# Kernel tuning notes

Measured on AMD Instinct MI355X. Metric: run time of the kernel, lower is better.

The kernel has to match this reference:

```python
import jax, jax.numpy as jnp
import numpy as np

S, Q, N, T, G = 20000, 32, 200000, 30, 64
D_IN, H, D_SV, D_LANG, D_FUSE = 300, 256, 64, 64, 128

def setup_inputs() -> dict:
    key = jax.random.key(0)
    ks = jax.random.split(key, 20)
    sc = 0.05
    inp = {
        'lang_feat': jax.random.normal(ks[0], (Q, T, D_IN), jnp.float32),
        'supvox_feat': jax.random.normal(ks[1], (S, D_SV), jnp.float32),
        'supvox_coords': jax.random.uniform(ks[2], (S, 3), jnp.float32),
        'lang_len': jax.random.randint(ks[3], (Q,), 5, T + 1).astype(jnp.int32),
        'grps': jax.random.randint(ks[4], (S,), 0, G).astype(jnp.int32),
        'supervox': jax.random.randint(ks[5], (N,), 0, S).astype(jnp.int32),
        'gt': jax.random.randint(ks[6], (N, Q), 0, 2).astype(jnp.int32),
        # GRU params (torch layout: [3H, in])
        'gru_w_ih': sc * jax.random.normal(ks[7], (3 * H, D_IN), jnp.float32),
        'gru_w_hh': sc * jax.random.normal(ks[8], (3 * H, H), jnp.float32),
        'gru_b_ih': sc * jax.random.normal(ks[9], (3 * H,), jnp.float32),
        'gru_b_hh': sc * jax.random.normal(ks[10], (3 * H,), jnp.float32),
        # lang_sqz: Linear(256,64) ReLU Linear(64,64)
        'sqz_w1': sc * jax.random.normal(ks[11], (D_LANG, H), jnp.float32),
        'sqz_b1': sc * jax.random.normal(ks[12], (D_LANG,), jnp.float32),
        'sqz_w2': sc * jax.random.normal(ks[13], (D_LANG, D_LANG), jnp.float32),
        'sqz_b2': sc * jax.random.normal(ks[14], (D_LANG,), jnp.float32),
        # feat_fuse: Linear(131,128) ReLU
        'fuse_w': sc * jax.random.normal(ks[15], (D_FUSE, D_SV + 3 + D_LANG), jnp.float32),
        'fuse_b': sc * jax.random.normal(ks[16], (D_FUSE,), jnp.float32),
        # heat_map: Linear(128,2) (Dropout = identity in eval)
        'heat_w': sc * jax.random.normal(ks[17], (2, D_FUSE), jnp.float32),
        'heat_b': sc * jax.random.normal(ks[18], (2,), jnp.float32),
    }
    return inp

def _gru_last(x, lens, w_ih, w_hh, b_ih, b_hh):
    # x: [Q, T, D_IN]; returns hidden at step lens[q]-1 (pack_padded_sequence semantics)
    def step(h, xt_t):
        xt, t = xt_t  # xt: [Q, D_IN]
        gi = xt @ w_ih.T + b_ih          # [Q, 3H]
        gh = h @ w_hh.T + b_hh           # [Q, 3H]
        ir, iz, inn = jnp.split(gi, 3, -1)
        hr, hz, hn = jnp.split(gh, 3, -1)
        r = jax.nn.sigmoid(ir + hr)
        z = jax.nn.sigmoid(iz + hz)
        n = jnp.tanh(inn + r * hn)
        h_new = (1.0 - z) * n + z * h
        h = jnp.where((t < lens)[:, None], h_new, h)
        return h, None
    h0 = jnp.zeros((x.shape[0], w_hh.shape[1]), x.dtype)
    hT, _ = jax.lax.scan(step, h0, (jnp.swapaxes(x, 0, 1), jnp.arange(x.shape[1])))
    return hT  # [Q, H]

def reference(lang_feat, supvox_feat, supvox_coords, lang_len, grps, supervox, gt,
              gru_w_ih, gru_w_hh, gru_b_ih, gru_b_hh,
              sqz_w1, sqz_b1, sqz_w2, sqz_b2, fuse_w, fuse_b, heat_w, heat_b):
    # language branch
    h = _gru_last(lang_feat, lang_len, gru_w_ih, gru_w_hh, gru_b_ih, gru_b_hh)  # [Q,H]
    lang = jax.nn.relu(h @ sqz_w1.T + sqz_b1) @ sqz_w2.T + sqz_b2               # [Q,64]
    # supervoxel branch: cat(feat, coords) -> [S,67]
    sv = jnp.concatenate([supvox_feat, supvox_coords], -1)
    # feat_fuse on cat(sv, lang): split the weight to avoid materializing [S,Q,131]
    d_sv = sv.shape[-1]
    sv_proj = sv @ fuse_w[:, :d_sv].T           # [S,128]
    lang_proj = lang @ fuse_w[:, d_sv:].T       # [Q,128]
    fused = jax.nn.relu(sv_proj[:, None, :] + lang_proj[None, :, :] + fuse_b)  # [S,Q,128]
    logits = fused @ heat_w.T + heat_b          # [S,Q,2]
    obj_score = jax.nn.softmax(logits, -1)[..., 1]  # [S,Q]
    # cluster-grouped mean score (grps_ one-hot; assumes unique(grps)==arange(G))
    grp_oh = (grps[:, None] == jnp.arange(G)).astype(obj_score.dtype)  # [S,G]
    grp_sum = jnp.einsum('sq,sg->qg', obj_score, grp_oh)               # [Q,G]
    sen_grp_score = grp_sum / grp_oh.sum(0)[None, :]                   # [Q,G]
    best = jnp.argmax(sen_grp_score, -1)        # [Q]
    supvox_sen = grp_oh[:, best]                # [S,Q] binary
    obj_pts = supvox_sen[supervox].astype(jnp.int32)  # [N,Q]
    inter = (obj_pts * gt).sum(0).astype(jnp.float32)
    union = jnp.bitwise_or(obj_pts, gt).sum(0).astype(jnp.float32)
    ious = inter / (union + 1e-5)               # [Q]
    return obj_pts, ious
```

## Files before the change

kernel.cpp:

```cpp
#include <hip/hip_runtime.h>
#include <hip/hip_bf16.h>
#include <math.h>

#define S_TOT 20000
#define Q_TOT 32
#define N_TOT 200000
#define T_MAX 30
#define G_TOT 64
#define D_IN 300
#define H_DIM 256
#define D_SV 64
#define D_LANG 64
#define D_FUSE 128
#define D_CAT 67
#define FW_LD 131
#define SCHUNK 32
#define NBLK3 (S_TOT / SCHUNK)
#define SENT64 0xFFFFFFFFFFFFFFFFull
#define PCHUNK 16
#define PTILES 40

#define GI_MT 32
#define GI_NT 64
#define GI_KC 100
#define GI_NB 12
#define GI_GRID (30 * GI_NB)
#define HG_ELEMS (30 * Q_TOT * H_DIM)

#define SYNCS_N 1024

__device__ __forceinline__ float sigmoidf_(float x) { return 1.0f / (1.0f + expf(-x)); }
__device__ __forceinline__ unsigned long long pack2(float a, float b) {
    return ((unsigned long long)__float_as_uint(b) << 32) | (unsigned long long)__float_as_uint(a);
}

__global__ __launch_bounds__(128) void k_gi(const float* __restrict__ lang_feat,
                                            const float* __restrict__ w_ih,
                                            const float* __restrict__ b_ih,
                                            const float* __restrict__ fuse_w,
                                            const float* __restrict__ sqz_w1,
                                            const float* __restrict__ sqz_w2,
                                            const float* __restrict__ heat_w,
                                            float* __restrict__ gi,
                                            float* __restrict__ fwt,
                                            float* __restrict__ w1t,
                                            float* __restrict__ w2t,
                                            float* __restrict__ wdr,
                                            float* __restrict__ hg,
                                            int* __restrict__ syncs) {
    const int tid = threadIdx.x;
    if (blockIdx.x >= GI_GRID) {
        const int xb = blockIdx.x - GI_GRID;
        if (xb == 0) {
            for (int i = tid; i < FW_LD * D_FUSE; i += 128)
                fwt[(i % FW_LD) * D_FUSE + (i / FW_LD)] = fuse_w[i];
            for (int i = tid; i < D_LANG * H_DIM; i += 128)
                w1t[(i & 255) * D_LANG + (i >> 8)] = sqz_w1[i];
            for (int i = tid; i < D_LANG * D_LANG; i += 128)
                w2t[(i & 63) * D_LANG + (i >> 6)] = sqz_w2[i];
            if (tid < D_FUSE) wdr[tid] = heat_w[D_FUSE + tid] - heat_w[tid];
        } else {
            const int fb = xb - 1;
            const int per4 = HG_ELEMS / 4 / 8;
            float4* dst = (float4*)hg + fb * per4;
            const float4 sv = make_float4(__uint_as_float(0xFFFFFFFFu), __uint_as_float(0xFFFFFFFFu),
                                          __uint_as_float(0xFFFFFFFFu), __uint_as_float(0xFFFFFFFFu));
            for (int i = tid; i < per4; i += 128) dst[i] = sv;
            if (fb == 0) for (int i = tid; i < SYNCS_N; i += 128) syncs[i] = 0;
        }
        return;
    }
    __shared__ float x_l[GI_KC][GI_MT + 1];
    __shared__ float w_l[GI_KC][GI_NT + 1];
    const int mb = blockIdx.x / GI_NB, nb = blockIdx.x % GI_NB;
    const int m0 = mb * GI_MT, n0 = nb * GI_NT;
    const int tq4 = (tid >> 4) * 4, jq4 = (tid & 15) * 4;

    float acc[4][4];
    #pragma unroll
    for (int i = 0; i < 4; ++i)
        #pragma unroll
        for (int j = 0; j < 4; ++j) acc[i][j] = 0.f;

    for (int kc = 0; kc < 3; ++kc) {
        const int k0 = kc * GI_KC;
        for (int i = tid; i < GI_MT * GI_KC; i += 128) {
            const int r = i / GI_KC, k = i % GI_KC;
            const int row = m0 + r, q = row / T_MAX, t = row - q * T_MAX;
            x_l[k][r] = lang_feat[(q * T_MAX + t) * D_IN + k0 + k];
        }
        for (int i = tid; i < GI_NT * GI_KC; i += 128) {
            const int r = i / GI_KC, k = i % GI_KC;
            w_l[k][r] = w_ih[(n0 + r) * D_IN + k0 + k];
        }
        __syncthreads();
        #pragma unroll 2
        for (int k = 0; k < GI_KC; ++k) {
            const float x0 = x_l[k][tq4 + 0], x1 = x_l[k][tq4 + 1];
            const float x2 = x_l[k][tq4 + 2], x3 = x_l[k][tq4 + 3];
            const float v0 = w_l[k][jq4 + 0], v1 = w_l[k][jq4 + 1];
            const float v2 = w_l[k][jq4 + 2], v3 = w_l[k][jq4 + 3];
            acc[0][0] = fmaf(x0, v0, acc[0][0]); acc[0][1] = fmaf(x0, v1, acc[0][1]);
            acc[0][2] = fmaf(x0, v2, acc[0][2]); acc[0][3] = fmaf(x0, v3, acc[0][3]);
            acc[1][0] = fmaf(x1, v0, acc[1][0]); acc[1][1] = fmaf(x1, v1, acc[1][1]);
            acc[1][2] = fmaf(x1, v2, acc[1][2]); acc[1][3] = fmaf(x1, v3, acc[1][3]);
            acc[2][0] = fmaf(x2, v0, acc[2][0]); acc[2][1] = fmaf(x2, v1, acc[2][1]);
            acc[2][2] = fmaf(x2, v2, acc[2][2]); acc[2][3] = fmaf(x2, v3, acc[2][3]);
            acc[3][0] = fmaf(x3, v0, acc[3][0]); acc[3][1] = fmaf(x3, v1, acc[3][1]);
            acc[3][2] = fmaf(x3, v2, acc[3][2]); acc[3][3] = fmaf(x3, v3, acc[3][3]);
        }
        __syncthreads();
    }
    const float b0 = b_ih[n0 + jq4 + 0], b1 = b_ih[n0 + jq4 + 1];
    const float b2 = b_ih[n0 + jq4 + 2], b3 = b_ih[n0 + jq4 + 3];
    #pragma unroll
    for (int i = 0; i < 4; ++i) {
        const int row = m0 + tq4 + i;
        const int q = row / T_MAX, t = row - q * T_MAX;
        float4 v = make_float4(acc[i][0] + b0, acc[i][1] + b1, acc[i][2] + b2, acc[i][3] + b3);
        *(float4*)&gi[(q * T_MAX + t) * 768 + n0 + jq4] = v;
    }
}

__global__ __launch_bounds__(384, 1) void k_gru8(const float* __restrict__ gi,
                                                 const float* __restrict__ w_hh,
                                                 const float* __restrict__ b_hh,
                                                 const int* __restrict__ lang_len,
                                                 float* __restrict__ hg,
                                                 float* __restrict__ hbuf,
                                                 const float* __restrict__ w1t,
                                                 const float* __restrict__ b1,
                                                 const float* __restrict__ w2t,
                                                 const float* __restrict__ b2,
                                                 const float* __restrict__ fwt,
                                                 const float* __restrict__ fuse_b,
                                                 float* __restrict__ langc,
                                                 int* __restrict__ qdone) {
    __shared__ __align__(16) float wlds[96 * 256];
    __shared__ __align__(16) float hlq[4 * 68];
    __shared__ float ghl[96];
    __shared__ float gil[T_MAX * 96];

    const int tid = threadIdx.x;
    const int q = blockIdx.x >> 3, b = blockIdx.x & 7;
    int len = lang_len[q]; if (len > T_MAX) len = T_MAX; if (len < 1) len = 1;

    {
        const float4* src4 = (const float4*)w_hh;
        float4* dst4 = (float4*)wlds;
        for (int i = tid; i < 96 * 64; i += 384) {
            const int r = i >> 6, c = i & 63;
            const int grow = ((r >> 5) << 8) + (b << 5) + (r & 31);
            dst4[r * 64 + (c ^ (r & 7))] = src4[grow * 64 + c];
        }
    }
    for (int i = tid; i < len * 96; i += 384) {
        const int t = i / 96, r = i % 96;
        gil[i] = gi[(q * T_MAX + t) * 768 + ((r >> 5) << 8) + (b << 5) + (r & 31)];
    }
    __syncthreads();

    float hfin = 0.f;
    {
        float hnew = 0.f;
        if (tid < 32) {
            const float bhr = b_hh[(b << 5) + tid];
            const float bhz = b_hh[H_DIM + (b << 5) + tid];
            const float bhn = b_hh[2 * H_DIM + (b << 5) + tid];
            const float r = sigmoidf_(gil[tid] + bhr);
            const float z = sigmoidf_(gil[32 + tid] + bhz);
            const float n = tanhf(gil[64 + tid] + r * bhn);
            hnew = (1.f - z) * n;
            if (len == 1) hfin = hnew;
        }
        if (tid < 64 && len > 1) {
            const float a0 = __shfl(hnew, 2 * (tid & 15));
            const float a1 = __shfl(hnew, 2 * (tid & 15) + 1);
            if (tid < 16) {
                unsigned long long* dst = (unsigned long long*)(hg + q * H_DIM + (b << 5));
                __hip_atomic_store(dst + tid, pack2(a0, a1), __ATOMIC_RELAXED, __HIP_MEMORY_SCOPE_AGENT);
            }
        }
    }

    const int row = tid >> 2, ql = tid & 3;
    const float bh = b_hh[((row >> 5) << 8) + (b << 5) + (row & 31)];
    const int rx = row & 7;
    const float4* wrow4 = (const float4*)wlds + row * 64;
    const int cbase = ql << 4;

    for (int t = 1; t < len; ++t) {
        if (tid < 128) {
            const unsigned long long* src =
                (const unsigned long long*)(hg + (size_t)(t - 1) * (Q_TOT * H_DIM) + q * H_DIM);
            unsigned long long v;
            while ((v = __hip_atomic_load(src + tid, __ATOMIC_RELAXED,
                                          __HIP_MEMORY_SCOPE_AGENT)) == SENT64)
                __builtin_amdgcn_s_sleep(1);
            const int k = 2 * tid;
            const int o = (k >> 6) * 68 + (k & 63);
            hlq[o]     = __uint_as_float((unsigned)(v & 0xffffffffu));
            hlq[o + 1] = __uint_as_float((unsigned)(v >> 32));
        }
        __syncthreads();
        float hold = 0.f;
        if (tid < 32) { const int k = (b << 5) + tid; hold = hlq[(k >> 6) * 68 + (k & 63)]; }
        const float4* h4 = (const float4*)(hlq + ql * 68);
        float ax = 0.f, ay = 0.f, az = 0.f, aw = 0.f;
        #pragma unroll
        for (int i = 0; i < 16; ++i) {
            const float4 wv = wrow4[(cbase + i) ^ rx];
            const float4 hv = h4[i];
            ax = fmaf(wv.x, hv.x, ax);
            ay = fmaf(wv.y, hv.y, ay);
            az = fmaf(wv.z, hv.z, az);
            aw = fmaf(wv.w, hv.w, aw);
        }
        float s = (ax + ay) + (az + aw);
        s += __shfl_xor(s, 1);
        s += __shfl_xor(s, 2);
        if (ql == 0) ghl[row] = s + bh;
        __syncthreads();
        float hnew = 0.f;
        if (tid < 32) {
            const float* gt_ = gil + t * 96;
            const float r = sigmoidf_(gt_[tid] + ghl[tid]);
            const float z = sigmoidf_(gt_[32 + tid] + ghl[32 + tid]);
            const float n = tanhf(gt_[64 + tid] + r * ghl[64 + tid]);
            hnew = (1.f - z) * n + z * hold;
            if (t == len - 1) hfin = hnew;
        }
        if (tid < 64 && t < len - 1) {
            const float a0 = __shfl(hnew, 2 * (tid & 15));
            const float a1 = __shfl(hnew, 2 * (tid & 15) + 1);
            if (tid < 16) {
                unsigned long long* dst =
                    (unsigned long long*)(hg + (size_t)t * (Q_TOT * H_DIM) + q * H_DIM + (b << 5));
                __hip_atomic_store(dst + tid, pack2(a0, a1), __ATOMIC_RELAXED, __HIP_MEMORY_SCOPE_AGENT);
            }
        }
    }

    if (tid < 32)
        __hip_atomic_store(&hbuf[q * H_DIM + (b << 5) + tid], hfin,
                           __ATOMIC_RELAXED, __HIP_MEMORY_SCOPE_AGENT);
    asm volatile("s_waitcnt vmcnt(0)" ::: "memory");
    __syncthreads();
    if (tid == 0)
        __hip_atomic_fetch_add(&qdone[q], 1, __ATOMIC_RELAXED, __HIP_MEMORY_SCOPE_AGENT);
    if (b != 0) return;

    if (tid == 0) {
        while (__hip_atomic_load(&qdone[q], __ATOMIC_RELAXED, __HIP_MEMORY_SCOPE_AGENT) < 8)
            __builtin_amdgcn_s_sleep(2);
    }
    __syncthreads();
    float* hql = gil;
    float* t1l = gil + 256;
    float* lgl = gil + 320;
    if (tid < H_DIM)
        hql[tid] = __hip_atomic_load(&hbuf[q * H_DIM + tid], __ATOMIC_RELAXED, __HIP_MEMORY_SCOPE_AGENT);
    __syncthreads();
    if (tid < 256) {
        const int c = tid >> 2, qq = tid & 3;
        float a = 0.f;
        #pragma unroll 8
        for (int j = 0; j < 64; ++j) {
            const int k = (qq << 6) + j;
            a = fmaf(w1t[k * D_LANG + c], hql[k], a);
        }
        a += __shfl_xor(a, 1);
        a += __shfl_xor(a, 2);
        if (qq == 0) t1l[c] = fmaxf(a + b1[c], 0.f);
    }
    __syncthreads();
    if (tid < 256) {
        const int c = tid >> 2, qq = tid & 3;
        float a = 0.f;
        #pragma unroll
        for (int j = 0; j < 16; ++j) {
            const int k = (qq << 4) + j;
            a = fmaf(w2t[k * D_LANG + c], t1l[k], a);
        }
        a += __shfl_xor(a, 1);
        a += __shfl_xor(a, 2);
        if (qq == 0) lgl[c] = a + b2[c];
    }
    __syncthreads();
    if (tid < 256) {
        const int d = tid >> 1, hh = tid & 1;
        float a = 0.f;
        #pragma unroll 8
        for (int j = 0; j < 32; ++j) {
            const int k = (hh << 5) + j;
            a = fmaf(fwt[(D_CAT + k) * D_FUSE + d], lgl[k], a);
        }
        a += __shfl_xor(a, 1);
        if (hh == 0) langc[q * D_FUSE + d] = a + fuse_b[d];
    }
}

__global__ __launch_bounds__(256, 3) void k_tail(const float* __restrict__ feat,
                                                 const float* __restrict__ coords,
                                                 const int* __restrict__ grps,
                                                 const float* __restrict__ langc,
                                                 const float* __restrict__ fwt,
                                                 const float* __restrict__ wdr_g,
                                                 const float* __restrict__ heat_b,
                                                 float* __restrict__ grp_part,
                                                 int* __restrict__ cnt_part,
                                                 float* __restrict__ grp2,
                                                 int* __restrict__ cnt2,
                                                 int* __restrict__ best,
                                                 const int* __restrict__ supervox,
                                                 const int* __restrict__ gt,
                                                 float* __restrict__ out,
                                                 int* __restrict__ syncs) {
    int* interG = syncs;
    int* unionG = syncs + 32;
    int* t_out  = syncs + 64;
    int* gtick  = syncs + 65;
    int* qtick  = syncs + 98;
    const int tid = threadIdx.x;
    const int bid = blockIdx.x;

    __shared__ __align__(16) float svin[SCHUNK][68];
    __shared__ __align__(16) float svp[SCHUNK][132];
    __shared__ float score[SCHUNK][Q_TOT];
    __shared__ int grps_l[SCHUNK];
    __shared__ float ps[4][G_TOT];
    __shared__ int   pc[4][G_TOT];
    __shared__ float sc[G_TOT];
    __shared__ int bl[Q_TOT];
    __shared__ int gm[G_TOT];
    __shared__ int bi_s[Q_TOT], bu_s[Q_TOT];
    __shared__ int islast;

    {
        const int s0 = bid * SCHUNK;
        const int dsl = tid & 7, q = tid >> 3;
        float lc[16], wdr[16];
        #pragma unroll
        for (int i = 0; i < 16; ++i) {
            const int d = dsl * 16 + i;
            lc[i]  = langc[q * D_FUSE + d];
            wdr[i] = wdr_g[d];
        }
        const float hbd = heat_b[1] - heat_b[0];

        for (int i = tid; i < SCHUNK * D_SV; i += 256) {
            const int r = i >> 6, c = i & 63;
            svin[r][c] = feat[(s0 + r) * D_SV + c];
        }
        if (tid < SCHUNK * 3) { const int r = tid / 3, c = tid % 3; svin[r][D_SV + c] = coords[(s0 + r) * 3 + c]; }
        if (tid < SCHUNK) grps_l[tid] = grps[s0 + tid];
        __syncthreads();

        {
            const int d = tid & 127, sl0 = tid >> 7;
            float acc[16];
            #pragma unroll
            for (int i = 0; i < 16; ++i) acc[i] = 0.f;
            for (int k4 = 0; k4 < 16; ++k4) {
                const float w0 = fwt[(4 * k4 + 0) * D_FUSE + d];
                const float w1 = fwt[(4 * k4 + 1) * D_FUSE + d];
                const float w2 = fwt[(4 * k4 + 2) * D_FUSE + d];
                const float w3 = fwt[(4 * k4 + 3) * D_FUSE + d];
                #pragma unroll
                for (int i = 0; i < 16; ++i) {
                    const float4 xv = *(const float4*)&svin[sl0 + 2 * i][4 * k4];
                    acc[i] = fmaf(xv.x, w0, fmaf(xv.y, w1, fmaf(xv.z, w2, fmaf(xv.w, w3, acc[i]))));
                }
            }
            for (int k = 64; k < D_CAT; ++k) {
                const float wv = fwt[k * D_FUSE + d];
                #pragma unroll
                for (int i = 0; i < 16; ++i)
                    acc[i] = fmaf(svin[sl0 + 2 * i][k], wv, acc[i]);
            }
            #pragma unroll
            for (int i = 0; i < 16; ++i) svp[sl0 + 2 * i][d] = acc[i];
        }
        __syncthreads();

        for (int sl = 0; sl < SCHUNK; ++sl) {
            const float4* sv4 = (const float4*)(&svp[sl][dsl * 16]);
            float part = 0.f;
            #pragma unroll
            for (int j = 0; j < 4; ++j) {
                const float4 v = sv4[j];
                part = fmaf(fmaxf(v.x + lc[4*j+0], 0.f), wdr[4*j+0], part);
                part = fmaf(fmaxf(v.y + lc[4*j+1], 0.f), wdr[4*j+1], part);
                part = fmaf(fmaxf(v.z + lc[4*j+2], 0.f), wdr[4*j+2], part);
                part = fmaf(fmaxf(v.w + lc[4*j+3], 0.f), wdr[4*j+3], part);
            }
            part += __shfl_xor(part, 1);
            part += __shfl_xor(part, 2);
            part += __shfl_xor(part, 4);
            if (dsl == 0) score[sl][q] = sigmoidf_(part + hbd);
        }
        __syncthreads();

        for (int i = 0; i < 8; ++i) {
            const int cell = tid + 256 * i;
            const int qq = cell >> 6, g = cell & 63;
            float sum = 0.f;
            #pragma unroll
            for (int sl = 0; sl < SCHUNK; ++sl)
                sum += (grps_l[sl] == g) ? score[sl][qq] : 0.f;
            __hip_atomic_store(&grp_part[bid * (Q_TOT * G_TOT) + cell], sum,
                               __ATOMIC_RELAXED, __HIP_MEMORY_SCOPE_AGENT);
            if (cell < G_TOT) {
                int c = 0;
                #pragma unroll
                for (int sl = 0; sl < SCHUNK; ++sl) c += (grps_l[sl] == g);
                __hip_atomic_store(&cnt_part[bid * G_TOT + g], c,
                                   __ATOMIC_RELAXED, __HIP_MEMORY_SCOPE_AGENT);
            }
        }
        asm volatile("s_waitcnt vmcnt(0)" ::: "memory");
        __syncthreads();
        if (tid == 0)
            __hip_atomic_fetch_add(&syncs[160 + 32 * (bid / PTILES)], 1,
                                   __ATOMIC_RELAXED, __HIP_MEMORY_SCOPE_AGENT);
    }

    if (bid < Q_TOT * PCHUNK) {
        const int q = bid & 31, c = bid >> 5;
        const int b0 = c * PTILES;
        int b1 = b0 + PTILES; if (b1 > NBLK3) b1 = NBLK3;
        if (tid == 0) {
            int* tc = &syncs[160 + 32 * c];
            const int tgt = b1 - b0;
            while (__hip_atomic_load(tc, __ATOMIC_RELAXED, __HIP_MEMORY_SCOPE_AGENT) < tgt)
                __builtin_amdgcn_s_sleep(4);
        }
        __syncthreads();
        const int bq = tid >> 6, g = tid & 63;
        float acc = 0.f; int cacc = 0;
        for (int b = b0 + bq; b < b1; b += 4) {
            acc  += grp_part[b * (Q_TOT * G_TOT) + q * G_TOT + g];
            cacc += cnt_part[b * G_TOT + g];
        }
        ps[bq][g] = acc; pc[bq][g] = cacc;
        __syncthreads();
        if (tid < G_TOT) {
            const float s = ((ps[0][tid] + ps[1][tid]) + ps[2][tid]) + ps[3][tid];
            const int  cc = ((pc[0][tid] + pc[1][tid]) + pc[2][tid]) + pc[3][tid];
            __hip_atomic_store(&grp2[(c * Q_TOT + q) * G_TOT + tid], s,
                               __ATOMIC_RELAXED, __HIP_MEMORY_SCOPE_AGENT);
            __hip_atomic_store(&cnt2[(c * Q_TOT + q) * G_TOT + tid], cc,
                               __ATOMIC_RELAXED, __HIP_MEMORY_SCOPE_AGENT);
        }
        __shared__ int myturn;
        asm volatile("s_waitcnt vmcnt(0)" ::: "memory");
        if (tid == 0) {
            const int old = __hip_atomic_fetch_add(&qtick[q], 1, __ATOMIC_RELAXED, __HIP_MEMORY_SCOPE_AGENT);
            myturn = (old == PCHUNK - 1) ? 1 : 0;
        }
        __syncthreads();
        if (myturn) {
            if (tid < G_TOT) {
                float s = 0.f; int cc = 0;
                #pragma unroll
                for (int c2 = 0; c2 < PCHUNK; ++c2) {
                    s  += grp2[(c2 * Q_TOT + q) * G_TOT + tid];
                    cc += cnt2[(c2 * Q_TOT + q) * G_TOT + tid];
                }
                sc[tid] = s / (float)cc;
            }
            __syncthreads();
            if (tid == 0) {
                float bv = sc[0]; int bi = 0;
                for (int g2 = 1; g2 < G_TOT; ++g2) if (sc[g2] > bv) { bv = sc[g2]; bi = g2; }
                __hip_atomic_store(&best[q], bi, __ATOMIC_RELAXED, __HIP_MEMORY_SCOPE_AGENT);
                asm volatile("s_waitcnt vmcnt(0)" ::: "memory");
                const int old = __hip_atomic_fetch_add(gtick, 1, __ATOMIC_RELAXED, __HIP_MEMORY_SCOPE_AGENT);
                if (old == Q_TOT - 1) {
                    #pragma unroll
                    for (int f = 0; f < 8; ++f)
                        __hip_atomic_store(&syncs[672 + 32 * f], 1,
                                           __ATOMIC_RELAXED, __HIP_MEMORY_SCOPE_AGENT);
                }
            }
        }
    }

    if (tid == 0) {
        int* fl = &syncs[672 + 32 * (bid & 7)];
        while (__hip_atomic_load(fl, __ATOMIC_RELAXED, __HIP_MEMORY_SCOPE_AGENT) == 0)
            __builtin_amdgcn_s_sleep(16);
    }
    __syncthreads();

    if (tid < Q_TOT) bl[tid] = best[tid];
    __syncthreads();
    if (tid < G_TOT) {
        int m = 0;
        #pragma unroll
        for (int qq = 0; qq < Q_TOT; ++qq) m |= (bl[qq] == tid) ? (1 << qq) : 0;
        gm[tid] = m;
    }
    __syncthreads();

    {
        const int gidx = bid * 256 + tid;
        const int q4 = (gidx & 7) * 4;
        const int nstride = (NBLK3 * 256) >> 3;
        int a0 = 0, a1 = 0, a2 = 0, a3 = 0;
        int u0 = 0, u1 = 0, u2 = 0, u3 = 0;
        for (int n = gidx >> 3; n < N_TOT; n += nstride) {
            const int m = gm[grps[supervox[n]]];
            const int4 g4 = *(const int4*)&gt[n * Q_TOT + q4];
            const int o0 = (m >> (q4 + 0)) & 1;
            const int o1 = (m >> (q4 + 1)) & 1;
            const int o2 = (m >> (q4 + 2)) & 1;
            const int o3 = (m >> (q4 + 3)) & 1;
            *(float4*)&out[n * Q_TOT + q4] =
                make_float4((float)o0, (float)o1, (float)o2, (float)o3);
            a0 += o0 & g4.x; u0 += o0 | g4.x;
            a1 += o1 & g4.y; u1 += o1 | g4.y;
            a2 += o2 & g4.z; u2 += o2 | g4.z;
            a3 += o3 & g4.w; u3 += o3 | g4.w;
        }
        if (tid < Q_TOT) { bi_s[tid] = 0; bu_s[tid] = 0; }
        __syncthreads();
        atomicAdd(&bi_s[q4 + 0], a0); atomicAdd(&bu_s[q4 + 0], u0);
        atomicAdd(&bi_s[q4 + 1], a1); atomicAdd(&bu_s[q4 + 1], u1);
        atomicAdd(&bi_s[q4 + 2], a2); atomicAdd(&bu_s[q4 + 2], u2);
        atomicAdd(&bi_s[q4 + 3], a3); atomicAdd(&bu_s[q4 + 3], u3);
        __syncthreads();
        if (tid < Q_TOT) { atomicAdd(&interG[tid], bi_s[tid]); atomicAdd(&unionG[tid], bu_s[tid]); }
        asm volatile("s_waitcnt vmcnt(0)" ::: "memory");
        if (tid == 0) {
            const int old = __hip_atomic_fetch_add(t_out, 1, __ATOMIC_RELAXED, __HIP_MEMORY_SCOPE_AGENT);
            islast = (old == NBLK3 - 1) ? 1 : 0;
        }
        __syncthreads();
        if (islast && tid < Q_TOT) {
            const int iv = __hip_atomic_load(&interG[tid], __ATOMIC_RELAXED, __HIP_MEMORY_SCOPE_AGENT);
            const int uv = __hip_atomic_load(&unionG[tid], __ATOMIC_RELAXED, __HIP_MEMORY_SCOPE_AGENT);
            out[(size_t)N_TOT * Q_TOT + tid] = (float)iv / ((float)uv + 1e-5f);
        }
    }
}

extern "C" void kernel_launch(void* const* d_in, const int* in_sizes, int n_in,
                              void* d_out, int out_size, void* d_ws, size_t ws_size,
                              hipStream_t stream) {
    const float* lang_feat = (const float*)d_in[0];
    const float* feat      = (const float*)d_in[1];
    const float* coords    = (const float*)d_in[2];
    const int*   lang_len  = (const int*)d_in[3];
    const int*   grps      = (const int*)d_in[4];
    const int*   supervox  = (const int*)d_in[5];
    const int*   gt        = (const int*)d_in[6];
    const float* w_ih      = (const float*)d_in[7];
    const float* w_hh      = (const float*)d_in[8];
    const float* b_ih      = (const float*)d_in[9];
    const float* b_hh      = (const float*)d_in[10];
    const float* sqz_w1    = (const float*)d_in[11];
    const float* sqz_b1    = (const float*)d_in[12];
    const float* sqz_w2    = (const float*)d_in[13];
    const float* sqz_b2    = (const float*)d_in[14];
    const float* fuse_w    = (const float*)d_in[15];
    const float* fuse_b    = (const float*)d_in[16];
    const float* heat_w    = (const float*)d_in[17];
    const float* heat_b    = (const float*)d_in[18];
    float* out = (float*)d_out;

    float* gi       = (float*)d_ws;
    float* hbuf     = gi + 737280;
    float* langc    = hbuf + 8192;
    float* grp_part = langc + 4096;
    int*   cnt_part = (int*)(grp_part + NBLK3 * 2048);
    int*   best     = cnt_part + NBLK3 * 64;
    int*   syncs    = best + 32;
    float* hg       = (float*)(syncs + SYNCS_N);
    float* fwt      = hg + HG_ELEMS;
    float* w1t      = fwt + FW_LD * D_FUSE;
    float* w2t      = w1t + H_DIM * D_LANG;
    float* wdr      = w2t + D_LANG * D_LANG;
    float* grp2     = wdr + 128;
    int*   cnt2     = (int*)(grp2 + PCHUNK * Q_TOT * G_TOT);

    k_gi   <<<GI_GRID + 9, 128, 0, stream>>>(lang_feat, w_ih, b_ih, fuse_w, sqz_w1, sqz_w2, heat_w,
                                             gi, fwt, w1t, w2t, wdr, hg, syncs);
    k_gru8 <<<Q_TOT * 8, 384, 0, stream>>>(gi, w_hh, b_hh, lang_len, hg, hbuf,
                                           w1t, sqz_b1, w2t, sqz_b2, fwt, fuse_b, langc,
                                           syncs + 66);
    k_tail <<<NBLK3, 256, 0, stream>>>(feat, coords, grps, langc, fwt, wdr, heat_b,
                                       grp_part, cnt_part, grp2, cnt2, best,
                                       supervox, gt, out, syncs);
}
```

Baseline: 202.7 us.

## Fuse input-projection GEMM, GRU and tail into one persistent mega-kernel

Measured after the change: 277.7 us. +37.0%, slower.

```diff
diff --git a/kernel.cpp b/kernel.cpp
--- a/kernel.cpp
+++ b/kernel.cpp
@@ -17,146 +17,138 @@
 #define SCHUNK 32
 #define NBLK3 (S_TOT / SCHUNK)
 #define SENT64 0xFFFFFFFFFFFFFFFFull
-#define PCHUNK 16
-#define PTILES 40
-
-#define GI_MT 32
-#define GI_NT 64
-#define GI_KC 100
-#define GI_NB 12
-#define GI_GRID (30 * GI_NB)
+#define PCHUNK 8
+#define PTILES 79
 #define HG_ELEMS (30 * Q_TOT * H_DIM)
-
-#define SYNCS_N 1024
+#define MEGA_GRID 256
+
+#define SYNCS_N 2048
 
 __device__ __forceinline__ float sigmoidf_(float x) { return 1.0f / (1.0f + expf(-x)); }
 __device__ __forceinline__ unsigned long long pack2(float a, float b) {
     return ((unsigned long long)__float_as_uint(b) << 32) | (unsigned long long)__float_as_uint(a);
 }
 
-__global__ __launch_bounds__(128) void k_gi(const float* __restrict__ lang_feat,
-                                            const float* __restrict__ w_ih,
-                                            const float* __restrict__ b_ih,
-                                            const float* __restrict__ fuse_w,
-                                            const float* __restrict__ sqz_w1,
-                                            const float* __restrict__ sqz_w2,
-                                            const float* __restrict__ heat_w,
-                                            float* __restrict__ gi,
-                                            float* __restrict__ fwt,
-                                            float* __restrict__ w1t,
-                                            float* __restrict__ w2t,
-                                            float* __restrict__ wdr,
-                                            float* __restrict__ hg,
-                                            int* __restrict__ syncs) {
+__global__ __launch_bounds__(128) void k_init(const float* __restrict__ fuse_w,
+                                              const float* __restrict__ sqz_w1,
+                                              const float* __restrict__ sqz_w2,
+                                              const float* __restrict__ heat_w,
+                                              float* __restrict__ fwt,
+                                              float* __restrict__ w1t,
+                                              float* __restrict__ w2t,
+                                              float* __restrict__ wdr,
+                                              float* __restrict__ hg,
+                                              int* __restrict__ syncs) {
     const int tid = threadIdx.x;
-    if (blockIdx.x >= GI_GRID) {
-        const int xb = blockIdx.x - GI_GRID;
-        if (xb == 0) {
-            for (int i = tid; i < FW_LD * D_FUSE; i += 128)
-                fwt[(i % FW_LD) * D_FUSE + (i / FW_LD)] = fuse_w[i];
-            for (int i = tid; i < D_LANG * H_DIM; i += 128)
-                w1t[(i & 255) * D_LANG + (i >> 8)] = sqz_w1[i];
-            for (int i = tid; i < D_LANG * D_LANG; i += 128)
-                w2t[(i & 63) * D_LANG + (i >> 6)] = sqz_w2[i];
-            if (tid < D_FUSE) wdr[tid] = heat_w[D_FUSE + tid] - heat_w[tid];
-        } else {
-            const int fb = xb - 1;
-            const int per4 = HG_ELEMS / 4 / 8;
-            float4* dst = (float4*)hg + fb * per4;
-            const float4 sv = make_float4(__uint_as_float(0xFFFFFFFFu), __uint_as_float(0xFFFFFFFFu),
-                                          __uint_as_float(0xFFFFFFFFu), __uint_as_float(0xFFFFFFFFu));
-            for (int i = tid; i < per4; i += 128) dst[i] = sv;
-            if (fb == 0) for (int i = tid; i < SYNCS_N; i += 128) syncs[i] = 0;
-        }
-        return;
-    }
-    __shared__ float x_l[GI_KC][GI_MT + 1];
-    __shared__ float w_l[GI_KC][GI_NT + 1];
-    const int mb = blockIdx.x / GI_NB, nb = blockIdx.x % GI_NB;
-    const int m0 = mb * GI_MT, n0 = nb * GI_NT;
-    const int tq4 = (tid >> 4) * 4, jq4 = (tid & 15) * 4;
-
-    float acc[4][4];
+    if (blockIdx.x == 0) {
+        for (int i = tid; i < FW_LD * D_FUSE; i += 128)
+            fwt[(i % FW_LD) * D_FUSE + (i / FW_LD)] = fuse_w[i];
+        for (int i = tid; i < D_LANG * H_DIM; i += 128)
+            w1t[(i & 255) * D_LANG + (i >> 8)] = sqz_w1[i];
+        for (int i = tid; i < D_LANG * D_LANG; i += 128)
+            w2t[(i & 63) * D_LANG + (i >> 6)] = sqz_w2[i];
+        if (tid < D_FUSE) wdr[tid] = heat_w[D_FUSE + tid] - heat_w[tid];
+    } else {
+        const int fb = blockIdx.x - 1;
+        const int per4 = HG_ELEMS / 4 / 8;
+        float4* dst = (float4*)hg + fb * per4;
+        const float4 sv = make_float4(__uint_as_float(0xFFFFFFFFu), __uint_as_float(0xFFFFFFFFu),
+                                      __uint_as_float(0xFFFFFFFFu), __uint_as_float(0xFFFFFFFFu));
+        for (int i = tid; i < per4; i += 128) dst[i] = sv;
+        if (fb == 0) for (int i = tid; i < SYNCS_N; i += 128) syncs[i] = 0;
+    }
+}
+
+__global__ __launch_bounds__(384, 1) void k_mega(
+    const float* __restrict__ lang_feat,
+    const float* __restrict__ w_ih, const float* __restrict__ b_ih,
+    const float* __restrict__ w_hh, const float* __restrict__ b_hh,
+    const int* __restrict__ lang_len,
+    float* __restrict__ hg, float* __restrict__ hbuf,
+    const float* __restrict__ w1t, const float* __restrict__ b1,
+    const float* __restrict__ w2t, const float* __restrict__ b2,
+    const float* __restrict__ fwt, const float* __restrict__ fuse_b,
+    float* __restrict__ langc,
+    const float* __restrict__ feat, const float* __restrict__ coords,
+    const int* __restrict__ grps, const float* __restrict__ wdr_g,
+    const float* __restrict__ heat_b,
+    float* __restrict__ grp_part, int* __restrict__ cnt_part,
+    float* __restrict__ grp2, int* __restrict__ cnt2,
+    int* __restrict__ best,
+    const int* __restrict__ supervox, const int* __restrict__ gt,
+    float* __restrict__ out, int* __restrict__ syncs)
+{
+    const int tid = threadIdx.x, bid = blockIdx.x;
+    const int q = bid >> 3, b = bid & 7;
+    int len = lang_len[q]; if (len > T_MAX) len = T_MAX; if (len < 1) len = 1;
+
+    __shared__ __align__(16) unsigned char SM[111360];
+    float* WL   = (float*)SM;
+    float* XL   = (float*)SM;
+    float* WcL  = (float*)(SM + 12480);
+    float* HLQ  = (float*)(SM + 98304);
+    float* GHL  = (float*)(SM + 99392);
+    float* GIL  = (float*)(SM + 99776);
+    float* SVIN = (float*)SM;
+    float* SVP  = (float*)(SM + 8704);
+    float* SCOREL = (float*)(SM + 25600);
+    int*   GRPSL  = (int*)(SM + 29696);
+    float* PS   = (float*)(SM + 29824);
+    int*   PC   = (int*)(SM + 30848);
+    float* SC   = (float*)(SM + 31872);
+    int*   BLs  = (int*)(SM + 32128);
+    int*   GMs  = (int*)(SM + 32256);
+    int*   BIS  = (int*)(SM + 32512);
+    int*   BUS  = (int*)(SM + 32640);
+    __shared__ int sflag1, sflag2;
+
+    const int r96 = tid >> 2, tg = tid & 3;
+    const int growI = ((r96 >> 5) << 8) + (b << 5) + (r96 & 31);
+    float gacc[8];
     #pragma unroll
-    for (int i = 0; i < 4; ++i)
+    for (int j = 0; j < 8; ++j) gacc[j] = 0.f;
+    for (int kc = 0; kc < 3; ++kc) {
+        const int k0 = kc * 100;
+        for (int i = tid; i < 3000; i += 384) {
+            const int t = i / 100, k = i - 100 * t;
+            XL[t * 104 + k] = lang_feat[(q * T_MAX + t) * D_IN + k0 + k];
+        }
+        for (int i = tid; i < 9600; i += 384) {
+            const int rr = i / 100, k = i - 100 * rr;
+            WcL[rr * 104 + k] =
+                w_ih[(size_t)(((rr >> 5) << 8) + (b << 5) + (rr & 31)) * D_IN + k0 + k];
+        }
+        __syncthreads();
+        for (int k4 = 0; k4 < 25; ++k4) {
+            const float4 wv = *(const float4*)&WcL[r96 * 104 + 4 * k4];
+            #pragma unroll
+            for (int j = 0; j < 8; ++j) {
+                const int t = tg + 4 * j;
+                if (t < 30) {
+                    const float4 xv = *(const float4*)&XL[t * 104 + 4 * k4];
+                    gacc[j] = fmaf(wv.x, xv.x, fmaf(wv.y, xv.y,
+                              fmaf(wv.z, xv.z, fmaf(wv.w, xv.w, gacc[j]))));
+                }
+            }
+        }
+        __syncthreads();
+    }
+    {
+        const float bih = b_ih[growI];
         #pragma unroll
-        for (int j = 0; j < 4; ++j) acc[i][j] = 0.f;
-
-    for (int kc = 0; kc < 3; ++kc) {
-        const int k0 = kc * GI_KC;
-        for (int i = tid; i < GI_MT * GI_KC; i += 128) {
-            const int r = i / GI_KC, k = i % GI_KC;
-            const int row = m0 + r, q = row / T_MAX, t = row - q * T_MAX;
-            x_l[k][r] = lang_feat[(q * T_MAX + t) * D_IN + k0 + k];
-        }
-        for (int i = tid; i < GI_NT * GI_KC; i += 128) {
-            const int r = i / GI_KC, k = i % GI_KC;
-            w_l[k][r] = w_ih[(n0 + r) * D_IN + k0 + k];
-        }
-        __syncthreads();
-        #pragma unroll 2
-        for (int k = 0; k < GI_KC; ++k) {
-            const float x0 = x_l[k][tq4 + 0], x1 = x_l[k][tq4 + 1];
-            const float x2 = x_l[k][tq4 + 2], x3 = x_l[k][tq4 + 3];
-            const float v0 = w_l[k][jq4 + 0], v1 = w_l[k][jq4 + 1];
-            const float v2 = w_l[k][jq4 + 2], v3 = w_l[k][jq4 + 3];
-            acc[0][0] = fmaf(x0, v0, acc[0][0]); acc[0][1] = fmaf(x0, v1, acc[0][1]);
-            acc[0][2] = fmaf(x0, v2, acc[0][2]); acc[0][3] = fmaf(x0, v3, acc[0][3]);
-            acc[1][0] = fmaf(x1, v0, acc[1][0]); acc[1][1] = fmaf(x1, v1, acc[1][1]);
-            acc[1][2] = fmaf(x1, v2, acc[1][2]); acc[1][3] = fmaf(x1, v3, acc[1][3]);
-            acc[2][0] = fmaf(x2, v0, acc[2][0]); acc[2][1] = fmaf(x2, v1, acc[2][1]);
-            acc[2][2] = fmaf(x2, v2, acc[2][2]); acc[2][3] = fmaf(x2, v3, acc[2][3]);
-            acc[3][0] = fmaf(x3, v0, acc[3][0]); acc[3][1] = fmaf(x3, v1, acc[3][1]);
-            acc[3][2] = fmaf(x3, v2, acc[3][2]); acc[3][3] = fmaf(x3, v3, acc[3][3]);
-        }
-        __syncthreads();
-    }
-    const float b0 = b_ih[n0 + jq4 + 0], b1 = b_ih[n0 + jq4 + 1];
-    const float b2 = b_ih[n0 + jq4 + 2], b3 = b_ih[n0 + jq4 + 3];
-    #pragma unroll
-    for (int i = 0; i < 4; ++i) {
-        const int row = m0 + tq4 + i;
-        const int q = row / T_MAX, t = row - q * T_MAX;
-        float4 v = make_float4(acc[i][0] + b0, acc[i][1] + b1, acc[i][2] + b2, acc[i][3] + b3);
-        *(float4*)&gi[(q * T_MAX + t) * 768 + n0 + jq4] = v;
-    }
-}
-
-__global__ __launch_bounds__(384, 1) void k_gru8(const float* __restrict__ gi,
-                                                 const float* __restrict__ w_hh,
-                                                 const float* __restrict__ b_hh,
-                                                 const int* __restrict__ lang_len,
-                                                 float* __restrict__ hg,
-                                                 float* __restrict__ hbuf,
-                                                 const float* __restrict__ w1t,
-                                                 const float* __restrict__ b1,
-                                                 const float* __restrict__ w2t,
-                                                 const float* __restrict__ b2,
-                                                 const float* __restrict__ fwt,
-                                                 const float* __restrict__ fuse_b,
-                                                 float* __restrict__ langc,
-                                                 int* __restrict__ qdone) {
-    __shared__ __align__(16) float wlds[96 * 256];
-    __shared__ __align__(16) float hlq[4 * 68];
-    __shared__ float ghl[96];
-    __shared__ float gil[T_MAX * 96];
-
-    const int tid = threadIdx.x;
-    const int q = blockIdx.x >> 3, b = blockIdx.x & 7;
-    int len = lang_len[q]; if (len > T_MAX) len = T_MAX; if (len < 1) len = 1;
-
+        for (int j = 0; j < 8; ++j) {
+            const int t = tg + 4 * j;
+            if (t < 30) GIL[t * 96 + r96] = gacc[j] + bih;
+        }
+    }
     {
         const float4* src4 = (const float4*)w_hh;
-        float4* dst4 = (float4*)wlds;
+        float4* dst4 = (float4*)WL;
         for (int i = tid; i < 96 * 64; i += 384) {
-            const int r = i >> 6, c = i & 63;
-            const int grow = ((r >> 5) << 8) + (b << 5) + (r & 31);
-            dst4[r * 64 + (c ^ (r & 7))] = src4[grow * 64 + c];
-        }
-    }
-    for (int i = tid; i < len * 96; i += 384) {
-        const int t = i / 96, r = i % 96;
-        gil[i] = gi[(q * T_MAX + t) * 768 + ((r >> 5) << 8) + (b << 5) + (r & 31)];
+            const int rr = i >> 6, c = i & 63;
+            const int grow = ((rr >> 5) << 8) + (b << 5) + (rr & 31);
+            dst4[rr * 64 + (c ^ (rr & 7))] = src4[grow * 64 + c];
+        }
     }
     __syncthreads();
 
@@ -167,9 +159,9 @@
             const float bhr = b_hh[(b << 5) + tid];
             const float bhz = b_hh[H_DIM + (b << 5) + tid];
             const float bhn = b_hh[2 * H_DIM + (b << 5) + tid];
-            const float r = sigmoidf_(gil[tid] + bhr);
-            const float z = sigmoidf_(gil[32 + tid] + bhz);
-            const float n = tanhf(gil[64 + tid] + r * bhn);
+            const float r = sigmoidf_(GIL[tid] + bhr);
+            const float z = sigmoidf_(GIL[32 + tid] + bhz);
+            const float n = tanhf(GIL[64 + tid] + r * bhn);
             hnew = (1.f - z) * n;
             if (len == 1) hfin = hnew;
         }
@@ -182,304 +174,290 @@
             }
         }
     }
-
-    const int row = tid >> 2, ql = tid & 3;
-    const float bh = b_hh[((row >> 5) << 8) + (b << 5) + (row & 31)];
-    const int rx = row & 7;
-    const float4* wrow4 = (const float4*)wlds + row * 64;
-    const int cbase = ql << 4;
-
-    for (int t = 1; t < len; ++t) {
-        if (tid < 128) {
-            const unsigned long long* src =
-                (const unsigned long long*)(hg + (size_t)(t - 1) * (Q_TOT * H_DIM) + q * H_DIM);
-            unsigned long long v;
-            while ((v = __hip_atomic_load(src + tid, __ATOMIC_RELAXED,
-                                          __HIP_MEMORY_SCOPE_AGENT)) == SENT64)
-                __builtin_amdgcn_s_sleep(1);
-            const int k = 2 * tid;
-            const int o = (k >> 6) * 68 + (k & 63);
-            hlq[o]     = __uint_as_float((unsigned)(v & 0xffffffffu));
-            hlq[o + 1] = __uint_as_float((unsigned)(v >> 32));
-        }
-        __syncthreads();
-        float hold = 0.f;
-        if (tid < 32) { const int k = (b << 5) + tid; hold = hlq[(k >> 6) * 68 + (k & 63)]; }
-        const float4* h4 = (const float4*)(hlq + ql * 68);
-        float ax = 0.f, ay = 0.f, az = 0.f, aw = 0.f;
-        #pragma unroll
-        for (int i = 0; i < 16; ++i) {
-            const float4 wv = wrow4[(cbase + i) ^ rx];
-            const float4 hv = h4[i];
-            ax = fmaf(wv.x, hv.x, ax);
-            ay = fmaf(wv.y, hv.y, ay);
-            az = fmaf(wv.z, hv.z, az);
-            aw = fmaf(wv.w, hv.w, aw);
-        }
-        float s = (ax + ay) + (az + aw);
-        s += __shfl_xor(s, 1);
-        s += __shfl_xor(s, 2);
-        if (ql == 0) ghl[row] = s + bh;
-        __syncthreads();
-        float hnew = 0.f;
-        if (tid < 32) {
-            const float* gt_ = gil + t * 96;
-            const float r = sigmoidf_(gt_[tid] + ghl[tid]);
-            const float z = sigmoidf_(gt_[32 + tid] + ghl[32 + tid]);
-            const float n = tanhf(gt_[64 + tid] + r * ghl[64 + tid]);
-            hnew = (1.f - z) * n + z * hold;
-            if (t == len - 1) hfin = hnew;
-        }
-        if (tid < 64 && t < len - 1) {
-            const float a0 = __shfl(hnew, 2 * (tid & 15));
-            const float a1 = __shfl(hnew, 2 * (tid & 15) + 1);
-            if (tid < 16) {
-                unsigned long long* dst =
-                    (unsigned long long*)(hg + (size_t)t * (Q_TOT * H_DIM) + q * H_DIM + (b << 5));
-                __hip_atomic_store(dst + tid, pack2(a0, a1), __ATOMIC_RELAXED, __HIP_MEMORY_SCOPE_AGENT);
-            }
-        }
-    }
-
+    {
+        const int row = tid >> 2, ql = tid & 3;
+        const float bh = b_hh[((row >> 5) << 8) + (b << 5) + (row & 31)];
+        const int rx = row & 7;
+        const float4* wrow4 = (const float4*)WL + row * 64;
+        const int cbase = ql << 4;
+        for (int t = 1; t < len; ++t) {
+            if (tid < 128) {
+                const unsigned long long* src =
+                    (const unsigned long long*)(hg + (size_t)(t - 1) * (Q_TOT * H_DIM) + q * H_DIM);
+                unsigned long long v;
+                while ((v = __hip_atomic_load(src + tid, __ATOMIC_RELAXED,
+                                              __HIP_MEMORY_SCOPE_AGENT)) == SENT64)
+                    __builtin_amdgcn_s_sleep(1);
+                const int k = 2 * tid;
+                const int o = (k >> 6) * 68 + (k & 63);
+                HLQ[o]     = __uint_as_float((unsigned)(v & 0xffffffffu));
+                HLQ[o + 1] = __uint_as_float((unsigned)(v >> 32));
+            }
+            __syncthreads();
+            float hold = 0.f;
+            if (tid < 32) { const int k = (b << 5) + tid; hold = HLQ[(k >> 6) * 68 + (k & 63)]; }
+            const float4* h4 = (const float4*)(HLQ + ql * 68);
+            float ax = 0.f, ay = 0.f, az = 0.f, aw = 0.f;
+            #pragma unroll
+            for (int i = 0; i < 16; ++i) {
+                const float4 wv = wrow4[(cbase + i) ^ rx];
+                const float4 hv = h4[i];
+                ax = fmaf(wv.x, hv.x, ax);
+                ay = fmaf(wv.y, hv.y, ay);
+                az = fmaf(wv.z, hv.z, az);
+                aw = fmaf(wv.w, hv.w, aw);
+            }
+            float s = (ax + ay) + (az + aw);
+            s += __shfl_xor(s, 1);
+            s += __shfl_xor(s, 2);
+            if (ql == 0) GHL[row] = s + bh;
+            __syncthreads();
+            float hnew = 0.f;
+            if (tid < 32) {
+                const float* gt_ = GIL + t * 96;
+                const float r = sigmoidf_(gt_[tid] + GHL[tid]);
+                const float z = sigmoidf_(gt_[32 + tid] + GHL[32 + tid]);
+                const float n = tanhf(gt_[64 + tid] + r * GHL[64 + tid]);
+                hnew = (1.f - z) * n + z * hold;
+                if (t == len - 1) hfin = hnew;
+            }
+            if (tid < 64 && t < len - 1) {
+                const float a0 = __shfl(hnew, 2 * (tid & 15));
+                const float a1 = __shfl(hnew, 2 * (tid & 15) + 1);
+                if (tid < 16) {
+                    unsigned long long* dst =
+                        (unsigned long long*)(hg + (size_t)t * (Q_TOT * H_DIM) + q * H_DIM + (b << 5));
+                    __hip_atomic_store(dst + tid, pack2(a0, a1), __ATOMIC_RELAXED, __HIP_MEMORY_SCOPE_AGENT);
+                }
+            }
+        }
+    }
     if (tid < 32)
         __hip_atomic_store(&hbuf[q * H_DIM + (b << 5) + tid], hfin,
                            __ATOMIC_RELAXED, __HIP_MEMORY_SCOPE_AGENT);
     asm volatile("s_waitcnt vmcnt(0)" ::: "memory");
     __syncthreads();
     if (tid == 0)
-        __hip_atomic_fetch_add(&qdone[q], 1, __ATOMIC_RELAXED, __HIP_MEMORY_SCOPE_AGENT);
-    if (b != 0) return;
-
+        __hip_atomic_fetch_add(&syncs[128 + 32 * q], 1, __ATOMIC_RELAXED, __HIP_MEMORY_SCOPE_AGENT);
+
+    if (b == 0) {
+        if (tid == 0) {
+            while (__hip_atomic_load(&syncs[128 + 32 * q], __ATOMIC_RELAXED, __HIP_MEMORY_SCOPE_AGENT) < 8)
+                __builtin_amdgcn_s_sleep(2);
+        }
+        __syncthreads();
+        float* hql = GIL;
+        float* t1l = GIL + 256;
+        float* lgl = GIL + 320;
+        if (tid < H_DIM)
+            hql[tid] = __hip_atomic_load(&hbuf[q * H_DIM + tid], __ATOMIC_RELAXED, __HIP_MEMORY_SCOPE_AGENT);
+        __syncthreads();
+        if (tid < 256) {
+            const int c = tid >> 2, qq = tid & 3;
+            float a = 0.f;
+            #pragma unroll 8
+            for (int j = 0; j < 64; ++j) {
+                const int k = (qq << 6) + j;
+                a = fmaf(w1t[k * D_LANG + c], hql[k], a);
+            }
+            a += __shfl_xor(a, 1);
+            a += __shfl_xor(a, 2);
+            if (qq == 0) t1l[c] = fmaxf(a + b1[c], 0.f);
+        }
+        __syncthreads();
+        if (tid < 256) {
+            const int c = tid >> 2, qq = tid & 3;
+            float a = 0.f;
+            #pragma unroll
+            for (int j = 0; j < 16; ++j) {
+                const int k = (qq << 4) + j;
+                a = fmaf(w2t[k * D_LANG + c], t1l[k], a);
+            }
+            a += __shfl_xor(a, 1);
+            a += __shfl_xor(a, 2);
+            if (qq == 0) lgl[c] = a + b2[c];
+        }
+        __syncthreads();
+        if (tid < 256) {
+            const int d = tid >> 1, hh = tid & 1;
+            float a = 0.f;
+            #pragma unroll 8
+            for (int j = 0; j < 32; ++j) {
+                const int k = (hh << 5) + j;
+                a = fmaf(fwt[(D_CAT + k) * D_FUSE + d], lgl[k], a);
+            }
+            a += __shfl_xor(a, 1);
+            if (hh == 0)
+                __hip_atomic_store(&langc[q * D_FUSE + d], a + fuse_b[d],
+                                   __ATOMIC_RELAXED, __HIP_MEMORY_SCOPE_AGENT);
+        }
+        asm volatile("s_waitcnt vmcnt(0)" ::: "memory");
+        __syncthreads();
+        if (tid == 0) {
+            const int old = __hip_atomic_fetch_add(&syncs[65], 1, __ATOMIC_RELAXED, __HIP_MEMORY_SCOPE_AGENT);
+            if (old == Q_TOT - 1) {
+                #pragma unroll
+                for (int f = 0; f < 8; ++f)
+                    __hip_atomic_store(&syncs[1408 + 32 * f], 1, __ATOMIC_RELAXED, __HIP_MEMORY_SCOPE_AGENT);
+            }
+        }
+    }
     if (tid == 0) {
-        while (__hip_atomic_load(&qdone[q], __ATOMIC_RELAXED, __HIP_MEMORY_SCOPE_AGENT) < 8)
-            __builtin_amdgcn_s_sleep(2);
+        int* fl = &syncs[1408 + 32 * (bid & 7)];
+        while (__hip_atomic_load(fl, __ATOMIC_RELAXED, __HIP_MEMORY_SCOPE_AGENT) == 0)
+            __builtin_amdgcn_s_sleep(8);
     }
     __syncthreads();
-    float* hql = gil;
-    float* t1l = gil + 256;
-    float* lgl = gil + 320;
-    if (tid < H_DIM)
-        hql[tid] = __hip_atomic_load(&hbuf[q * H_DIM + tid], __ATOMIC_RELAXED, __HIP_MEMORY_SCOPE_AGENT);
-    __syncthreads();
-    if (tid < 256) {
-        const int c = tid >> 2, qq = tid & 3;
-        float a = 0.f;
-        #pragma unroll 8
-        for (int j = 0; j < 64; ++j) {
-            const int k = (qq << 6) + j;
-            a = fmaf(w1t[k * D_LANG + c], hql[k], a);
-        }
-        a += __shfl_xor(a, 1);
-        a += __shfl_xor(a, 2);
-        if (qq == 0) t1l[c] = fmaxf(a + b1[c], 0.f);
-    }
-    __syncthreads();
-    if (tid < 256) {
-        const int c = tid >> 2, qq = tid & 3;
-        float a = 0.f;
-        #pragma unroll
-        for (int j = 0; j < 16; ++j) {
-            const int k = (qq << 4) + j;
-            a = fmaf(w2t[k * D_LANG + c], t1l[k], a);
-        }
-        a += __shfl_xor(a, 1);
-        a += __shfl_xor(a, 2);
-        if (qq == 0) lgl[c] = a + b2[c];
-    }
-    __syncthreads();
-    if (tid < 256) {
-        const int d = tid >> 1, hh = tid & 1;
-        float a = 0.f;
-        #pragma unroll 8
-        for (int j = 0; j < 32; ++j) {
-            const int k = (hh << 5) + j;
-            a = fmaf(fwt[(D_CAT + k) * D_FUSE + d], lgl[k], a);
-        }
-        a += __shfl_xor(a, 1);
-        if (hh == 0) langc[q * D_FUSE + d] = a + fuse_b[d];
-    }
-}
-
-__global__ __launch_bounds__(256, 3) void k_tail(const float* __restrict__ feat,
-                                                 const float* __restrict__ coords,
-                                                 const int* __restrict__ grps,
-                                                 const float* __restrict__ langc,
-                                                 const float* __restrict__ fwt,
-                                                 const float* __restrict__ wdr_g,
-                                                 const float* __restrict__ heat_b,
-                                                 float* __restrict__ grp_part,
-                                                 int* __restrict__ cnt_part,
-                                                 float* __restrict__ grp2,
-                                                 int* __restrict__ cnt2,
-                                                 int* __restrict__ best,
-                                                 const int* __restrict__ supervox,
-                                                 const int* __restrict__ gt,
-                                                 float* __restrict__ out,
-                                                 int* __restrict__ syncs) {
-    int* interG = syncs;
-    int* unionG = syncs + 32;
-    int* t_out  = syncs + 64;
-    int* gtick  = syncs + 65;
-    int* qtick  = syncs + 98;
-    const int tid = threadIdx.x;
-    const int bid = blockIdx.x;
-
-    __shared__ __align__(16) float svin[SCHUNK][68];
-    __shared__ __align__(16) float svp[SCHUNK][132];
-    __shared__ float score[SCHUNK][Q_TOT];
-    __shared__ int grps_l[SCHUNK];
-    __shared__ float ps[4][G_TOT];
-    __shared__ int   pc[4][G_TOT];
-    __shared__ float sc[G_TOT];
-    __shared__ int bl[Q_TOT];
-    __shared__ int gm[G_TOT];
-    __shared__ int bi_s[Q_TOT], bu_s[Q_TOT];
-    __shared__ int islast;
-
-    {
-        const int s0 = bid * SCHUNK;
-        const int dsl = tid & 7, q = tid >> 3;
+
+    {
+        const int dsl = tid & 7, qf = tid >> 3;
         float lc[16], wdr[16];
-        #pragma unroll
-        for (int i = 0; i < 16; ++i) {
-            const int d = dsl * 16 + i;
-            lc[i]  = langc[q * D_FUSE + d];
-            wdr[i] = wdr_g[d];
+        if (tid < 256) {
+            #pragma unroll
+            for (int i = 0; i < 16; ++i) {
+                const int d = dsl * 16 + i;
+                lc[i]  = langc[qf * D_FUSE + d];
+                wdr[i] = wdr_g[d];
+            }
         }
         const float hbd = heat_b[1] - heat_b[0];
 
-        for (int i = tid; i < SCHUNK * D_SV; i += 256) {
-            const int r = i >> 6, c = i & 63;
-            svin[r][c] = feat[(s0 + r) * D_SV + c];
-        }
-        if (tid < SCHUNK * 3) { const int r = tid / 3, c = tid % 3; svin[r][D_SV + c] = coords[(s0 + r) * 3 + c]; }
-        if (tid < SCHUNK) grps_l[tid] = grps[s0 + tid];
-        __syncthreads();
-
-        {
-            const int d = tid & 127, sl0 = tid >> 7;
-            float acc[16];
-            #pragma unroll
-            for (int i = 0; i < 16; ++i) acc[i] = 0.f;
-            for (int k4 = 0; k4 < 16; ++k4) {
-                const float w0 = fwt[(4 * k4 + 0) * D_FUSE + d];
-                const float w1 = fwt[(4 * k4 + 1) * D_FUSE + d];
-                const float w2 = fwt[(4 * k4 + 2) * D_FUSE + d];
-                const float w3 = fwt[(4 * k4 + 3) * D_FUSE + d];
+        for (int tile = bid; tile < NBLK3; tile += MEGA_GRID) {
+            const int s0 = tile * SCHUNK;
+            __syncthreads();
+            for (int i = tid; i < SCHUNK * D_SV; i += 384) {
+                const int r = i >> 6, c = i & 63;
+                SVIN[r * 68 + c] = feat[(s0 + r) * D_SV + c];
+            }
+            if (tid < SCHUNK * 3) { const int r = tid / 3, c = tid % 3; SVIN[r * 68 + D_SV + c] = coords[(s0 + r) * 3 + c]; }
+            if (tid < SCHUNK) GRPSL[tid] = grps[s0 + tid];
+            __syncthreads();
+            if (tid < 256) {
+                const int d = tid & 127, sl0 = tid >> 7;
+                float acc[16];
                 #pragma unroll
-                for (int i = 0; i < 16; ++i) {
-                    const float4 xv = *(const float4*)&svin[sl0 + 2 * i][4 * k4];
-                    acc[i] = fmaf(xv.x, w0, fmaf(xv.y, w1, fmaf(xv.z, w2, fmaf(xv.w, w3, acc[i]))));
-                }
-            }
-            for (int k = 64; k < D_CAT; ++k) {
-                const float wv = fwt[k * D_FUSE + d];
+                for (int i = 0; i < 16; ++i) acc[i] = 0.f;
+                for (int k4 = 0; k4 < 16; ++k4) {
+                    const float w0 = fwt[(4 * k4 + 0) * D_FUSE + d];
+                    const float w1 = fwt[(4 * k4 + 1) * D_FUSE + d];
+                    const float w2 = fwt[(4 * k4 + 2) * D_FUSE + d];
+                    const float w3 = fwt[(4 * k4 + 3) * D_FUSE + d];
+                    #pragma unroll
+                    for (int i = 0; i < 16; ++i) {
+                        const float4 xv = *(const float4*)&SVIN[(sl0 + 2 * i) * 68 + 4 * k4];
+                        acc[i] = fmaf(xv.x, w0, fmaf(xv.y, w1, fmaf(xv.z, w2, fmaf(xv.w, w3, acc[i]))));
+                    }
+                }
+                for (int k = 64; k < D_CAT; ++k) {
+                    const float wv = fwt[k * D_FUSE + d];
+                    #pragma unroll
+                    for (int i = 0; i < 16; ++i)
+                        acc[i] = fmaf(SVIN[(sl0 + 2 * i) * 68 + k], wv, acc[i]);
+                }
                 #pragma unroll
-                for (int i = 0; i < 16; ++i)
-                    acc[i] = fmaf(svin[sl0 + 2 * i][k], wv, acc[i]);
-            }
-            #pragma unroll
-            for (int i = 0; i < 16; ++i) svp[sl0 + 2 * i][d] = acc[i];
-        }
-        __syncthreads();
-
-        for (int sl = 0; sl < SCHUNK; ++sl) {
-            const float4* sv4 = (const float4*)(&svp[sl][dsl * 16]);
-            float part = 0.f;
-            #pragma unroll
-            for (int j = 0; j < 4; ++j) {
-                const float4 v = sv4[j];
-                part = fmaf(fmaxf(v.x + lc[4*j+0], 0.f), wdr[4*j+0], part);
-                part = fmaf(fmaxf(v.y + lc[4*j+1], 0.f), wdr[4*j+1], part);
-                part = fmaf(fmaxf(v.z + lc[4*j+2], 0.f), wdr[4*j+2], part);
-                part = fmaf(fmaxf(v.w + lc[4*j+3], 0.f), wdr[4*j+3], part);
-            }
-            part += __shfl_xor(part, 1);
-            part += __shfl_xor(part, 2);
-            part += __shfl_xor(part, 4);
-            if (dsl == 0) score[sl][q] = sigmoidf_(part + hbd);
-        }
-        __syncthreads();
-
-        for (int i = 0; i < 8; ++i) {
-            const int cell = tid + 256 * i;
-            const int qq = cell >> 6, g = cell & 63;
-            float sum = 0.f;
-            #pragma unroll
-            for (int sl = 0; sl < SCHUNK; ++sl)
-                sum += (grps_l[sl] == g) ? score[sl][qq] : 0.f;
-            __hip_atomic_store(&grp_part[bid * (Q_TOT * G_TOT) + cell], sum,
-                               __ATOMIC_RELAXED, __HIP_MEMORY_SCOPE_AGENT);
-            if (cell < G_TOT) {
-                int c = 0;
+                for (int i = 0; i < 16; ++i) SVP[(sl0 + 2 * i) * 132 + d] = acc[i];
+            }
+            __syncthreads();
+            if (tid < 256) {
+                for (int sl = 0; sl < SCHUNK; ++sl) {
+                    const float4* sv4 = (const float4*)(&SVP[sl * 132 + dsl * 16]);
+                    float part = 0.f;
+                    #pragma unroll
+                    for (int j = 0; j < 4; ++j) {
+                        const float4 v = sv4[j];
+                        part = fmaf(fmaxf(v.x + lc[4*j+0], 0.f), wdr[4*j+0], part);
+                        part = fmaf(fmaxf(v.y + lc[4*j+1], 0.f), wdr[4*j+1], part);
+                        part = fmaf(fmaxf(v.z + lc[4*j+2], 0.f), wdr[4*j+2], part);
+                        part = fmaf(fmaxf(v.w + lc[4*j+3], 0.f), wdr[4*j+3], part);
+                    }
+                    part += __shfl_xor(part, 1);
+                    part += __shfl_xor(part, 2);
+                    part += __shfl_xor(part, 4);
+                    if (dsl == 0) SCOREL[sl * 32 + qf] = sigmoidf_(part + hbd);
+                }
+            }
+            __syncthreads();
+            for (int cell = tid; cell < Q_TOT * G_TOT; cell += 384) {
+                const int qq = cell >> 6, g = cell & 63;
+                float sum = 0.f;
                 #pragma unroll
-                for (int sl = 0; sl < SCHUNK; ++sl) c += (grps_l[sl] == g);
-                __hip_atomic_store(&cnt_part[bid * G_TOT + g], c,
+                for (int sl = 0; sl < SCHUNK; ++sl)
+                    sum += (GRPSL[sl] == g) ? SCOREL[sl * 32 + qq] : 0.f;
+                __hip_atomic_store(&grp_part[tile * (Q_TOT * G_TOT) + cell], sum,
                                    __ATOMIC_RELAXED, __HIP_MEMORY_SCOPE_AGENT);
-            }
-        }
-        asm volatile("s_waitcnt vmcnt(0)" ::: "memory");
-        __syncthreads();
-        if (tid == 0)
-            __hip_atomic_fetch_add(&syncs[160 + 32 * (bid / PTILES)], 1,
-                                   __ATOMIC_RELAXED, __HIP_MEMORY_SCOPE_AGENT);
-    }
-
-    if (bid < Q_TOT * PCHUNK) {
-        const int q = bid & 31, c = bid >> 5;
-        const int b0 = c * PTILES;
+                if (cell < G_TOT) {
+                    int c = 0;
+                    #pragma unroll
+                    for (int sl = 0; sl < SCHUNK; ++sl) c += (GRPSL[sl] == g);
+                    __hip_atomic_store(&cnt_part[tile * G_TOT + g], c,
+                                       __ATOMIC_RELAXED, __HIP_MEMORY_SCOPE_AGENT);
+                }
+            }
+            asm volatile("s_waitcnt vmcnt(0)" ::: "memory");
+            __syncthreads();
+            if (tid == 0)
+                __hip_atomic_fetch_add(&syncs[1152 + 32 * (tile / PTILES)], 1,
+                                       __ATOMIC_RELAXED, __HIP_MEMORY_SCOPE_AGENT);
+        }
+    }
+
+    {
+        const int qa = bid & 31, ca = bid >> 5;
+        const int b0 = ca * PTILES;
         int b1 = b0 + PTILES; if (b1 > NBLK3) b1 = NBLK3;
         if (tid == 0) {
-            int* tc = &syncs[160 + 32 * c];
+            int* tc = &syncs[1152 + 32 * ca];
             const int tgt = b1 - b0;
             while (__hip_atomic_load(tc, __ATOMIC_RELAXED, __HIP_MEMORY_SCOPE_AGENT) < tgt)
                 __builtin_amdgcn_s_sleep(4);
         }
         __syncthreads();
-        const int bq = tid >> 6, g = tid & 63;
-        float acc = 0.f; int cacc = 0;
-        for (int b = b0 + bq; b < b1; b += 4) {
-            acc  += grp_part[b * (Q_TOT * G_TOT) + q * G_TOT + g];
-            cacc += cnt_part[b * G_TOT + g];
-        }
-        ps[bq][g] = acc; pc[bq][g] = cacc;
+        if (tid < 256) {
+            const int bq = tid >> 6, g = tid & 63;
+            float acc = 0.f; int cacc = 0;
+            for (int bb = b0 + bq; bb < b1; bb += 4) {
+                acc  += grp_part[bb * (Q_TOT * G_TOT) + qa * G_TOT + g];
+                cacc += cnt_part[bb * G_TOT + g];
+            }
+            PS[bq * 64 + g] = acc; PC[bq * 64 + g] = cacc;
+        }
         __syncthreads();
         if (tid < G_TOT) {
-            const float s = ((ps[0][tid] + ps[1][tid]) + ps[2][tid]) + ps[3][tid];
-            const int  cc = ((pc[0][tid] + pc[1][tid]) + pc[2][tid]) + pc[3][tid];
-            __hip_atomic_store(&grp2[(c * Q_TOT + q) * G_TOT + tid], s,
+            const float s = ((PS[tid] + PS[64 + tid]) + PS[128 + tid]) + PS[192 + tid];
+            const int  cc = ((PC[tid] + PC[64 + tid]) + PC[128 + tid]) + PC[192 + tid];
+            __hip_atomic_store(&grp2[(ca * Q_TOT + qa) * G_TOT + tid], s,
                                __ATOMIC_RELAXED, __HIP_MEMORY_SCOPE_AGENT);
-            __hip_atomic_store(&cnt2[(c * Q_TOT + q) * G_TOT + tid], cc,
+            __hip_atomic_store(&cnt2[(ca * Q_TOT + qa) * G_TOT + tid], cc,
                                __ATOMIC_RELAXED, __HIP_MEMORY_SCOPE_AGENT);
         }
-        __shared__ int myturn;
         asm volatile("s_waitcnt vmcnt(0)" ::: "memory");
         if (tid == 0) {
-            const int old = __hip_atomic_fetch_add(&qtick[q], 1, __ATOMIC_RELAXED, __HIP_MEMORY_SCOPE_AGENT);
-            myturn = (old == PCHUNK - 1) ? 1 : 0;
-        }
-        __syncthreads();
-        if (myturn) {
+            const int old = __hip_atomic_fetch_add(&syncs[129 + 32 * qa], 1,
+                                                   __ATOMIC_RELAXED, __HIP_MEMORY_SCOPE_AGENT);
+            sflag1 = (old == PCHUNK - 1) ? 1 : 0;
+        }
+        __syncthreads();
+        if (sflag1) {
             if (tid < G_TOT) {
                 float s = 0.f; int cc = 0;
                 #pragma unroll
                 for (int c2 = 0; c2 < PCHUNK; ++c2) {
-                    s  += grp2[(c2 * Q_TOT + q) * G_TOT + tid];
-                    cc += cnt2[(c2 * Q_TOT + q) * G_TOT + tid];
-                }
-                sc[tid] = s / (float)cc;
+                    s  += grp2[(c2 * Q_TOT + qa) * G_TOT + tid];
+                    cc += cnt2[(c2 * Q_TOT + qa) * G_TOT + tid];
+                }
+                SC[tid] = s / (float)cc;
             }
             __syncthreads();
             if (tid == 0) {
-                float bv = sc[0]; int bi = 0;
-                for (int g2 = 1; g2 < G_TOT; ++g2) if (sc[g2] > bv) { bv = sc[g2]; bi = g2; }
-                __hip_atomic_store(&best[q], bi, __ATOMIC_RELAXED, __HIP_MEMORY_SCOPE_AGENT);
+                float bv = SC[0]; int bi = 0;
+                for (int g2 = 1; g2 < G_TOT; ++g2) if (SC[g2] > bv) { bv = SC[g2]; bi = g2; }
+                __hip_atomic_store(&best[qa], bi, __ATOMIC_RELAXED, __HIP_MEMORY_SCOPE_AGENT);
                 asm volatile("s_waitcnt vmcnt(0)" ::: "memory");
-                const int old = __hip_atomic_fetch_add(gtick, 1, __ATOMIC_RELAXED, __HIP_MEMORY_SCOPE_AGENT);
+                const int old = __hip_atomic_fetch_add(&syncs[66], 1, __ATOMIC_RELAXED, __HIP_MEMORY_SCOPE_AGENT);
                 if (old == Q_TOT - 1) {
                     #pragma unroll
                     for (int f = 0; f < 8; ++f)
-                        __hip_atomic_store(&syncs[672 + 32 * f], 1,
+                        __hip_atomic_store(&syncs[1664 + 32 * f], 1,
                                            __ATOMIC_RELAXED, __HIP_MEMORY_SCOPE_AGENT);
                 }
             }
@@ -487,30 +465,29 @@
     }
 
     if (tid == 0) {
-        int* fl = &syncs[672 + 32 * (bid & 7)];
+        int* fl = &syncs[1664 + 32 * (bid & 7)];
         while (__hip_atomic_load(fl, __ATOMIC_RELAXED, __HIP_MEMORY_SCOPE_AGENT) == 0)
             __builtin_amdgcn_s_sleep(16);
     }
     __syncthreads();
-
-    if (tid < Q_TOT) bl[tid] = best[tid];
+    if (tid < Q_TOT) BLs[tid] = best[tid];
     __syncthreads();
     if (tid < G_TOT) {
         int m = 0;
         #pragma unroll
-        for (int qq = 0; qq < Q_TOT; ++qq) m |= (bl[qq] == tid) ? (1 << qq) : 0;
-        gm[tid] = m;
+        for (int qq = 0; qq < Q_TOT; ++qq) m |= (BLs[qq] == tid) ? (1 << qq) : 0;
+        GMs[tid] = m;
     }
     __syncthreads();
 
     {
-        const int gidx = bid * 256 + tid;
+        const int gidx = bid * 384 + tid;
         const int q4 = (gidx & 7) * 4;
-        const int nstride = (NBLK3 * 256) >> 3;
+        const int nstride = (MEGA_GRID * 384) >> 3;
         int a0 = 0, a1 = 0, a2 = 0, a3 = 0;
         int u0 = 0, u1 = 0, u2 = 0, u3 = 0;
         for (int n = gidx >> 3; n < N_TOT; n += nstride) {
-            const int m = gm[grps[supervox[n]]];
+            const int m = GMs[grps[supervox[n]]];
             const int4 g4 = *(const int4*)&gt[n * Q_TOT + q4];
             const int o0 = (m >> (q4 + 0)) & 1;
             const int o1 = (m >> (q4 + 1)) & 1;
@@ -523,23 +500,23 @@
             a2 += o2 & g4.z; u2 += o2 | g4.z;
             a3 += o3 & g4.w; u3 += o3 | g4.w;
         }
-        if (tid < Q_TOT) { bi_s[tid] = 0; bu_s[tid] = 0; }
-        __syncthreads();
-        atomicAdd(&bi_s[q4 + 0], a0); atomicAdd(&bu_s[q4 + 0], u0);
-        atomicAdd(&bi_s[q4 + 1], a1); atomicAdd(&bu_s[q4 + 1], u1);
-        atomicAdd(&bi_s[q4 + 2], a2); atomicAdd(&bu_s[q4 + 2], u2);
-        atomicAdd(&bi_s[q4 + 3], a3); atomicAdd(&bu_s[q4 + 3], u3);
-        __syncthreads();
-        if (tid < Q_TOT) { atomicAdd(&interG[tid], bi_s[tid]); atomicAdd(&unionG[tid], bu_s[tid]); }
+        if (tid < Q_TOT) { BIS[tid] = 0; BUS[tid] = 0; }
+        __syncthreads();
+        atomicAdd(&BIS[q4 + 0], a0); atomicAdd(&BUS[q4 + 0], u0);
+        atomicAdd(&BIS[q4 + 1], a1); atomicAdd(&BUS[q4 + 1], u1);
+        atomicAdd(&BIS[q4 + 2], a2); atomicAdd(&BUS[q4 + 2], u2);
+        atomicAdd(&BIS[q4 + 3], a3); atomicAdd(&BUS[q4 + 3], u3);
+        __syncthreads();
+        if (tid < Q_TOT) { atomicAdd(&syncs[tid], BIS[tid]); atomicAdd(&syncs[32 + tid], BUS[tid]); }
         asm volatile("s_waitcnt vmcnt(0)" ::: "memory");
         if (tid == 0) {
-            const int old = __hip_atomic_fetch_add(t_out, 1, __ATOMIC_RELAXED, __HIP_MEMORY_SCOPE_AGENT);
-            islast = (old == NBLK3 - 1) ? 1 : 0;
-        }
-        __syncthreads();
-        if (islast && tid < Q_TOT) {
-            const int iv = __hip_atomic_load(&interG[tid], __ATOMIC_RELAXED, __HIP_MEMORY_SCOPE_AGENT);
-            const int uv = __hip_atomic_load(&unionG[tid], __ATOMIC_RELAXED, __HIP_MEMORY_SCOPE_AGENT);
+            const int old = __hip_atomic_fetch_add(&syncs[64], 1, __ATOMIC_RELAXED, __HIP_MEMORY_SCOPE_AGENT);
+            sflag2 = (old == MEGA_GRID - 1) ? 1 : 0;
+        }
+        __syncthreads();
+        if (sflag2 && tid < Q_TOT) {
+            const int iv = __hip_atomic_load(&syncs[tid], __ATOMIC_RELAXED, __HIP_MEMORY_SCOPE_AGENT);
+            const int uv = __hip_atomic_load(&syncs[32 + tid], __ATOMIC_RELAXED, __HIP_MEMORY_SCOPE_AGENT);
             out[(size_t)N_TOT * Q_TOT + tid] = (float)iv / ((float)uv + 1e-5f);
         }
     }
@@ -569,8 +546,7 @@
     const float* heat_b    = (const float*)d_in[18];
     float* out = (float*)d_out;
 
-    float* gi       = (float*)d_ws;
-    float* hbuf     = gi + 737280;
+    float* hbuf     = (float*)d_ws;
     float* langc    = hbuf + 8192;
     float* grp_part = langc + 4096;
     int*   cnt_part = (int*)(grp_part + NBLK3 * 2048);
@@ -584,12 +560,11 @@
     float* grp2     = wdr + 128;
     int*   cnt2     = (int*)(grp2 + PCHUNK * Q_TOT * G_TOT);
 
-    k_gi   <<<GI_GRID + 9, 128, 0, stream>>>(lang_feat, w_ih, b_ih, fuse_w, sqz_w1, sqz_w2, heat_w,
-                                             gi, fwt, w1t, w2t, wdr, hg, syncs);
-    k_gru8 <<<Q_TOT * 8, 384, 0, stream>>>(gi, w_hh, b_hh, lang_len, hg, hbuf,
-                                           w1t, sqz_b1, w2t, sqz_b2, fwt, fuse_b, langc,
-                                           syncs + 66);
-    k_tail <<<NBLK3, 256, 0, stream>>>(feat, coords, grps, langc, fwt, wdr, heat_b,
-                                       grp_part, cnt_part, grp2, cnt2, best,
-                                       supervox, gt, out, syncs);
+    k_init<<<9, 128, 0, stream>>>(fuse_w, sqz_w1, sqz_w2, heat_w,
+                                  fwt, w1t, w2t, wdr, hg, syncs);
+    k_mega<<<MEGA_GRID, 384, 0, stream>>>(lang_feat, w_ih, b_ih, w_hh, b_hh, lang_len,
+                                          hg, hbuf, w1t, sqz_b1, w2t, sqz_b2, fwt, fuse_b, langc,
+                                          feat, coords, grps, wdr, heat_b,
+                                          grp_part, cnt_part, grp2, cnt2, best,
+                                          supervox, gt, out, syncs);
 }
```
